# Kernel tuning notes

Hardware: AMD Instinct MI355X
Metric: run time of the kernel (lower is better)

Reference implementation:

```python
import jax, jax.numpy as jnp
import numpy as np

B, S, D, E = 8, 1024, 2048, 2  # batch, seq, model_dim, num_experts

def setup_inputs() -> dict:
    key = jax.random.key(0)
    k0, k1, k2, k3 = jax.random.split(key, 4)
    x = jax.random.normal(k0, (B, S, D), dtype=jnp.float32)
    wg = jax.random.normal(k1, (D, E), dtype=jnp.float32) * 0.02          # gate projection
    W = jax.random.normal(k2, (E, D, D), dtype=jnp.float32) / np.sqrt(D)  # expert weights [E, in, out]
    b = jax.random.normal(k3, (E, D), dtype=jnp.float32) * 0.02           # expert biases
    return {"x": x, "wg": wg, "W": W, "b": b}

def reference(x, wg, W, b):
    # --- Top1 gate ---
    logits = jnp.einsum('bsd,de->bse', x, wg)          # [B,S,E]
    gates = jax.nn.softmax(logits, axis=-1)
    idx = jnp.argmax(gates, axis=-1)                   # [B,S] top-1 expert per token
    gate_val = jnp.max(gates, axis=-1)                 # [B,S] top-1 gate prob
    # --- Expert GEMMs (dense over the 2 experts, then select == dispatch+combine) ---
    expert_out = jnp.einsum('bsd,edh->ebsh', x, W) + b[:, None, None, :]  # [E,B,S,D]
    onehot = jax.nn.one_hot(idx, E, dtype=x.dtype)     # [B,S,E]
    moe_out = jnp.einsum('bse,ebsh->bsh', onehot, expert_out) * gate_val[..., None]  # [B,S,D]
    # --- einsum('ijk->ij') then log_softmax(dim=1) ---
    y = jnp.sum(moe_out, axis=-1)                      # [B,S]
    return jax.nn.log_softmax(y, axis=1)
```

## Files before the change

### kernel.cpp

```cpp
#include <hip/hip_runtime.h>

#define B_ 8
#define S_ 1024
#define D_ 2048
#define E_ 2

__device__ inline float wave_reduce_sum(float v) {
    #pragma unroll
    for (int off = 32; off > 0; off >>= 1) v += __shfl_down(v, off, 64);
    return v;
}
__device__ inline float wave_reduce_max(float v) {
    #pragma unroll
    for (int off = 32; off > 0; off >>= 1) v = fmaxf(v, __shfl_down(v, off, 64));
    return v;
}

__global__ __launch_bounds__(256) void reduce_rows_kernel(
        const float* __restrict__ W, const float* __restrict__ bvec,
        float* __restrict__ Wsum, float* __restrict__ bsum) {
    const int row = blockIdx.x;
    const float* src;
    float* dst;
    if (row < E_ * D_) { src = W + (size_t)row * D_;            dst = Wsum + row; }
    else               { src = bvec + (size_t)(row - E_ * D_) * D_; dst = bsum + (row - E_ * D_); }

    const float4* s4 = (const float4*)src;
    float s = 0.0f;
    for (int i = threadIdx.x; i < D_ / 4; i += 256) {
        float4 v = s4[i];
        s += v.x + v.y + v.z + v.w;
    }
    s = wave_reduce_sum(s);
    __shared__ float lds[4];
    const int wave = threadIdx.x >> 6, lane = threadIdx.x & 63;
    if (lane == 0) lds[wave] = s;
    __syncthreads();
    if (threadIdx.x == 0) *dst = lds[0] + lds[1] + lds[2] + lds[3];
}

__global__ __launch_bounds__(256) void token_kernel(
        const float* __restrict__ x, const float* __restrict__ wg,
        const float* __restrict__ Wsum, const float* __restrict__ bsum,
        float* __restrict__ y) {
    const int tok = blockIdx.x;
    const float4* x4  = (const float4*)(x + (size_t)tok * D_);
    const float4* w0  = (const float4*)(Wsum);
    const float4* w1  = (const float4*)(Wsum + D_);
    const float4* wg4 = (const float4*)(wg);

    float d0 = 0.0f, d1 = 0.0f, g0 = 0.0f, g1 = 0.0f;
    for (int i = threadIdx.x; i < D_ / 4; i += 256) {
        float4 xv = x4[i];
        float4 a  = w0[i];
        float4 c  = w1[i];
        float4 u  = wg4[2 * i];
        float4 v  = wg4[2 * i + 1];
        d0 += xv.x * a.x + xv.y * a.y + xv.z * a.z + xv.w * a.w;
        d1 += xv.x * c.x + xv.y * c.y + xv.z * c.z + xv.w * c.w;
        g0 += xv.x * u.x + xv.y * u.z + xv.z * v.x + xv.w * v.z;
        g1 += xv.x * u.y + xv.y * u.w + xv.z * v.y + xv.w * v.w;
    }
    d0 = wave_reduce_sum(d0);
    d1 = wave_reduce_sum(d1);
    g0 = wave_reduce_sum(g0);
    g1 = wave_reduce_sum(g1);

    __shared__ float lds[4][4];
    const int wave = threadIdx.x >> 6, lane = threadIdx.x & 63;
    if (lane == 0) { lds[wave][0] = d0; lds[wave][1] = d1; lds[wave][2] = g0; lds[wave][3] = g1; }
    __syncthreads();
    if (threadIdx.x == 0) {
        float D0 = lds[0][0] + lds[1][0] + lds[2][0] + lds[3][0];
        float D1 = lds[0][1] + lds[1][1] + lds[2][1] + lds[3][1];
        float G0 = lds[0][2] + lds[1][2] + lds[2][2] + lds[3][2];
        float G1 = lds[0][3] + lds[1][3] + lds[2][3] + lds[3][3];
        const int idx = (G1 > G0) ? 1 : 0;
        const float diff = idx ? (G0 - G1) : (G1 - G0);
        const float gate = 1.0f / (1.0f + __expf(diff) * 0.0f + expf(diff));
        const float dot  = idx ? D1 : D0;
        y[tok] = gate * (dot + bsum[idx]);
    }
}

__global__ __launch_bounds__(256) void logsoftmax_kernel(
        const float* __restrict__ y, float* __restrict__ out) {
    const int b = blockIdx.x;
    const float* row = y + (size_t)b * S_;
    float* orow = out + (size_t)b * S_;

    float m = -3.4e38f;
    for (int i = threadIdx.x; i < S_; i += 256) m = fmaxf(m, row[i]);
    m = wave_reduce_max(m);
    __shared__ float lds[4];
    __shared__ float M_s, L_s;
    const int wave = threadIdx.x >> 6, lane = threadIdx.x & 63;
    if (lane == 0) lds[wave] = m;
    __syncthreads();
    if (threadIdx.x == 0)
        M_s = fmaxf(fmaxf(lds[0], lds[1]), fmaxf(lds[2], lds[3]));
    __syncthreads();
    const float M = M_s;

    float s = 0.0f;
    for (int i = threadIdx.x; i < S_; i += 256) s += expf(row[i] - M);
    s = wave_reduce_sum(s);
    __syncthreads();
    if (lane == 0) lds[wave] = s;
    __syncthreads();
    if (threadIdx.x == 0)
        L_s = M + logf(lds[0] + lds[1] + lds[2] + lds[3]);
    __syncthreads();
    const float lse = L_s;

    for (int i = threadIdx.x; i < S_; i += 256) orow[i] = row[i] - lse;
}

extern "C" void kernel_launch(void* const* d_in, const int* in_sizes, int n_in,
                              void* d_out, int out_size, void* d_ws, size_t ws_size,
                              hipStream_t stream) {
    const float* x  = (const float*)d_in[0];
    const float* wg = (const float*)d_in[1];
    const float* W  = (const float*)d_in[2];
    const float* bv = (const float*)d_in[3];
    float* out = (float*)d_out;

    float* ws   = (float*)d_ws;
    float* Wsum = ws;
    float* bsum = ws + E_ * D_;
    float* y    = ws + E_ * D_ + 16;

    reduce_rows_kernel<<<E_ * D_ + E_, 256, 0, stream>>>(W, bv, Wsum, bsum);
    token_kernel<<<B_ * S_, 256, 0, stream>>>(x, wg, Wsum, bsum, y);
    logsoftmax_kernel<<<B_, 256, 0, stream>>>(y, out);
}
```

Measured before the change: 30.43 us.

## Map one row/token per wavefront and drop LDS reductions

Both the row-reduction and token kernels now give each wavefront its own row or token, not one per 256-thread block. This removes the LDS cross-wave reduction and the __syncthreads, and launches a quarter as many blocks. Streaming loads use nontemporal hints, and the loops are fully unrolled. The log-softmax kernel keeps one float4 per thread in registers across its three passes, so it no longer re-reads y.

```diff
diff --git a/kernel.cpp b/kernel.cpp
--- a/kernel.cpp
+++ b/kernel.cpp
@@ -4,6 +4,9 @@
 #define S_ 1024
 #define D_ 2048
 #define E_ 2
+#define NROWS (E_ * D_ + E_)
+
+typedef float f32x4 __attribute__((ext_vector_type(4)));
 
 __device__ inline float wave_reduce_sum(float v) {
     #pragma unroll
@@ -19,43 +22,45 @@
 __global__ __launch_bounds__(256) void reduce_rows_kernel(
         const float* __restrict__ W, const float* __restrict__ bvec,
         float* __restrict__ Wsum, float* __restrict__ bsum) {
-    const int row = blockIdx.x;
-    const float* src;
-    float* dst;
-    if (row < E_ * D_) { src = W + (size_t)row * D_;            dst = Wsum + row; }
-    else               { src = bvec + (size_t)(row - E_ * D_) * D_; dst = bsum + (row - E_ * D_); }
-
-    const float4* s4 = (const float4*)src;
+    const int wave = threadIdx.x >> 6, lane = threadIdx.x & 63;
+    const int row = blockIdx.x * 4 + wave;
+    if (row >= NROWS) return;
+    const float* src = (row < E_ * D_) ? (W + (size_t)row * D_)
+                                       : (bvec + (size_t)(row - E_ * D_) * D_);
+    const f32x4* s4 = (const f32x4*)src;
     float s = 0.0f;
-    for (int i = threadIdx.x; i < D_ / 4; i += 256) {
-        float4 v = s4[i];
-        s += v.x + v.y + v.z + v.w;
+    #pragma unroll
+    for (int j = 0; j < D_ / 4 / 64; ++j) {
+        f32x4 v = __builtin_nontemporal_load(&s4[lane + j * 64]);
+        s += (v.x + v.y) + (v.z + v.w);
     }
     s = wave_reduce_sum(s);
-    __shared__ float lds[4];
-    const int wave = threadIdx.x >> 6, lane = threadIdx.x & 63;
-    if (lane == 0) lds[wave] = s;
-    __syncthreads();
-    if (threadIdx.x == 0) *dst = lds[0] + lds[1] + lds[2] + lds[3];
+    if (lane == 0) {
+        if (row < E_ * D_) Wsum[row] = s;
+        else               bsum[row - E_ * D_] = s;
+    }
 }
 
 __global__ __launch_bounds__(256) void token_kernel(
         const float* __restrict__ x, const float* __restrict__ wg,
         const float* __restrict__ Wsum, const float* __restrict__ bsum,
         float* __restrict__ y) {
-    const int tok = blockIdx.x;
-    const float4* x4  = (const float4*)(x + (size_t)tok * D_);
-    const float4* w0  = (const float4*)(Wsum);
-    const float4* w1  = (const float4*)(Wsum + D_);
-    const float4* wg4 = (const float4*)(wg);
+    const int wave = threadIdx.x >> 6, lane = threadIdx.x & 63;
+    const int tok = blockIdx.x * 4 + wave;
+    const f32x4* x4  = (const f32x4*)(x + (size_t)tok * D_);
+    const f32x4* w0  = (const f32x4*)(Wsum);
+    const f32x4* w1  = (const f32x4*)(Wsum + D_);
+    const f32x4* wg4 = (const f32x4*)(wg);
 
     float d0 = 0.0f, d1 = 0.0f, g0 = 0.0f, g1 = 0.0f;
-    for (int i = threadIdx.x; i < D_ / 4; i += 256) {
-        float4 xv = x4[i];
-        float4 a  = w0[i];
-        float4 c  = w1[i];
-        float4 u  = wg4[2 * i];
-        float4 v  = wg4[2 * i + 1];
+    #pragma unroll
+    for (int j = 0; j < D_ / 4 / 64; ++j) {
+        const int i = lane + j * 64;
+        f32x4 xv = __builtin_nontemporal_load(&x4[i]);
+        f32x4 a  = w0[i];
+        f32x4 c  = w1[i];
+        f32x4 u  = wg4[2 * i];
+        f32x4 v  = wg4[2 * i + 1];
         d0 += xv.x * a.x + xv.y * a.y + xv.z * a.z + xv.w * a.w;
         d1 += xv.x * c.x + xv.y * c.y + xv.z * c.z + xv.w * c.w;
         g0 += xv.x * u.x + xv.y * u.z + xv.z * v.x + xv.w * v.z;
@@ -66,19 +71,11 @@
     g0 = wave_reduce_sum(g0);
     g1 = wave_reduce_sum(g1);
 
-    __shared__ float lds[4][4];
-    const int wave = threadIdx.x >> 6, lane = threadIdx.x & 63;
-    if (lane == 0) { lds[wave][0] = d0; lds[wave][1] = d1; lds[wave][2] = g0; lds[wave][3] = g1; }
-    __syncthreads();
-    if (threadIdx.x == 0) {
-        float D0 = lds[0][0] + lds[1][0] + lds[2][0] + lds[3][0];
-        float D1 = lds[0][1] + lds[1][1] + lds[2][1] + lds[3][1];
-        float G0 = lds[0][2] + lds[1][2] + lds[2][2] + lds[3][2];
-        float G1 = lds[0][3] + lds[1][3] + lds[2][3] + lds[3][3];
-        const int idx = (G1 > G0) ? 1 : 0;
-        const float diff = idx ? (G0 - G1) : (G1 - G0);
-        const float gate = 1.0f / (1.0f + __expf(diff) * 0.0f + expf(diff));
-        const float dot  = idx ? D1 : D0;
+    if (lane == 0) {
+        const int idx = (g1 > g0) ? 1 : 0;
+        const float diff = idx ? (g0 - g1) : (g1 - g0);
+        const float gate = 1.0f / (1.0f + expf(diff));
+        const float dot  = idx ? d1 : d0;
         y[tok] = gate * (dot + bsum[idx]);
     }
 }
@@ -86,11 +83,10 @@
 __global__ __launch_bounds__(256) void logsoftmax_kernel(
         const float* __restrict__ y, float* __restrict__ out) {
     const int b = blockIdx.x;
-    const float* row = y + (size_t)b * S_;
-    float* orow = out + (size_t)b * S_;
+    const f32x4* row4 = (const f32x4*)(y + (size_t)b * S_);
+    f32x4 v = row4[threadIdx.x];
 
-    float m = -3.4e38f;
-    for (int i = threadIdx.x; i < S_; i += 256) m = fmaxf(m, row[i]);
+    float m = fmaxf(fmaxf(v.x, v.y), fmaxf(v.z, v.w));
     m = wave_reduce_max(m);
     __shared__ float lds[4];
     __shared__ float M_s, L_s;
@@ -102,8 +98,7 @@
     __syncthreads();
     const float M = M_s;
 
-    float s = 0.0f;
-    for (int i = threadIdx.x; i < S_; i += 256) s += expf(row[i] - M);
+    float s = expf(v.x - M) + expf(v.y - M) + expf(v.z - M) + expf(v.w - M);
     s = wave_reduce_sum(s);
     __syncthreads();
     if (lane == 0) lds[wave] = s;
@@ -113,7 +108,9 @@
     __syncthreads();
     const float lse = L_s;
 
-    for (int i = threadIdx.x; i < S_; i += 256) orow[i] = row[i] - lse;
+    f32x4 o;
+    o.x = v.x - lse; o.y = v.y - lse; o.z = v.z - lse; o.w = v.w - lse;
+    ((f32x4*)(out + (size_t)b * S_))[threadIdx.x] = o;
 }
 
 extern "C" void kernel_launch(void* const* d_in, const int* in_sizes, int n_in,
@@ -130,7 +127,7 @@
     float* bsum = ws + E_ * D_;
     float* y    = ws + E_ * D_ + 16;
 
-    reduce_rows_kernel<<<E_ * D_ + E_, 256, 0, stream>>>(W, bv, Wsum, bsum);
-    token_kernel<<<B_ * S_, 256, 0, stream>>>(x, wg, Wsum, bsum, y);
+    reduce_rows_kernel<<<(NROWS + 3) / 4, 256, 0, stream>>>(W, bv, Wsum, bsum);
+    token_kernel<<<B_ * S_ / 4, 256, 0, stream>>>(x, wg, Wsum, bsum, y);
     logsoftmax_kernel<<<B_, 256, 0, stream>>>(y, out);
 }
```

New measurement: 30.70 us. Within noise of the previous version (+0.9%).
